# Performance work log

Measured on AMD Instinct MI355X. Metric: run time of the kernel, lower is better.

The kernel has to match this reference:

```python
import jax, jax.numpy as jnp
import numpy as np

DIM = 640
HEADS = 8
HEAD_DIM = 80
CROSS = 768
FF_INNER = 4 * DIM  # 2560
EPS = 1e-5
SCALE = HEAD_DIM ** -0.5


def _ln(x, w, b):
    m = jnp.mean(x, axis=-1, keepdims=True)
    v = jnp.var(x, axis=-1, keepdims=True)
    return (x - m) * jax.lax.rsqrt(v + EPS) * w + b


def _split_heads(x):  # [B,S,D] -> [B,H,S,dh]
    B, S, D = x.shape
    return x.reshape(B, S, HEADS, D // HEADS).transpose(0, 2, 1, 3)


def _merge_heads(x):  # [B,H,S,dh] -> [B,S,D]
    B, H, S, dh = x.shape
    return x.transpose(0, 2, 1, 3).reshape(B, S, H * dh)


def _mha(q, k, v):
    # q:[B,S,D] k,v:[B,Skv,D]
    qh, kh, vh = _split_heads(q), _split_heads(k), _split_heads(v)
    scores = jnp.einsum('bhqd,bhkd->bhqk', qh, kh) * SCALE
    probs = jax.nn.softmax(scores, axis=-1)
    out = jnp.einsum('bhqk,bhkd->bhqd', probs, vh)
    return _merge_heads(out)


def _forward(hidden_states, encoder_hidden_states, video_length, p):
    BF, S, D = hidden_states.shape
    f = video_length
    b = BF // f

    # ---- attn1: sparse causal self-attention ----
    x = _ln(hidden_states, p['ln1_w'], p['ln1_b'])
    q = x @ p['q1']
    k = x @ p['k1']
    v = x @ p['v1']
    former = jnp.concatenate([jnp.zeros((1,), jnp.int32), jnp.arange(f - 1, dtype=jnp.int32)])
    def gather_kv(t):  # [BF,S,D] -> [BF,2S,D]
        t = t.reshape(b, f, S, D)
        first = jnp.broadcast_to(t[:, 0:1], (b, f, S, D))
        prev = t[:, former]
        return jnp.concatenate([first, prev], axis=2).reshape(BF, 2 * S, D)
    k = gather_kv(k)
    v = gather_kv(v)
    attn1 = _mha(q, k, v) @ p['o1_w'] + p['o1_b']
    hidden_states = attn1 + hidden_states

    # ---- attn2: cross attention to text ----
    x = _ln(hidden_states, p['ln2_w'], p['ln2_b'])
    q = x @ p['q2']
    k = encoder_hidden_states @ p['k2']
    v = encoder_hidden_states @ p['v2']
    attn2 = _mha(q, k, v) @ p['o2_w'] + p['o2_b']
    hidden_states = attn2 + hidden_states

    # ---- feed-forward (geglu) ----
    x = _ln(hidden_states, p['ln3_w'], p['ln3_b'])
    proj = x @ p['ff_w1'] + p['ff_b1']
    h, gate = jnp.split(proj, 2, axis=-1)
    ff = (h * jax.nn.gelu(gate)) @ p['ff_w2'] + p['ff_b2']
    return ff + hidden_states


def setup_inputs() -> dict:
    key = jax.random.key(0)
    ks = jax.random.split(key, 20)
    s = lambda i, shape, scale=0.02: jax.random.normal(ks[i], shape, jnp.float32) * scale
    inp = {
        'hidden_states': jax.random.normal(ks[0], (8, 1024, DIM), jnp.float32),
        'encoder_hidden_states': jax.random.normal(ks[1], (8, 77, CROSS), jnp.float32),
        'video_length': 8,
        'ln1_w': jnp.ones((DIM,)), 'ln1_b': jnp.zeros((DIM,)),
        'q1': s(2, (DIM, DIM)), 'k1': s(3, (DIM, DIM)), 'v1': s(4, (DIM, DIM)),
        'o1_w': s(5, (DIM, DIM)), 'o1_b': jnp.zeros((DIM,)),
        'ln2_w': jnp.ones((DIM,)), 'ln2_b': jnp.zeros((DIM,)),
        'q2': s(6, (DIM, DIM)), 'k2': s(7, (CROSS, DIM)), 'v2': s(8, (CROSS, DIM)),
        'o2_w': s(9, (DIM, DIM)), 'o2_b': jnp.zeros((DIM,)),
        'ln3_w': jnp.ones((DIM,)), 'ln3_b': jnp.zeros((DIM,)),
        'ff_w1': s(10, (DIM, 2 * FF_INNER)), 'ff_b1': jnp.zeros((2 * FF_INNER,)),
        'ff_w2': s(11, (FF_INNER, DIM)), 'ff_b2': jnp.zeros((DIM,)),
    }
    return inp


def reference(hidden_states, encoder_hidden_states, video_length,
              ln1_w, ln1_b, q1, k1, v1, o1_w, o1_b,
              ln2_w, ln2_b, q2, k2, v2, o2_w, o2_b,
              ln3_w, ln3_b, ff_w1, ff_b1, ff_w2, ff_b2):
    p = dict(ln1_w=ln1_w, ln1_b=ln1_b, q1=q1, k1=k1, v1=v1, o1_w=o1_w, o1_b=o1_b,
             ln2_w=ln2_w, ln2_b=ln2_b, q2=q2, k2=k2, v2=v2, o2_w=o2_w, o2_b=o2_b,
             ln3_w=ln3_w, ln3_b=ln3_b, ff_w1=ff_w1, ff_b1=ff_b1, ff_w2=ff_w2, ff_b2=ff_b2)
    return _forward(hidden_states, encoder_hidden_states, video_length, p)
```

## Files before the change

kernel.cpp:

```cpp
#include <hip/hip_runtime.h>
#include <stdint.h>

#define TOK   8192
#define DIM   640
#define HEADS 8
#define HD    80
#define SEQ   1024
#define CROSS 768
#define ETOK  616
#define FFI   2560
#define SCALE 0.11180339887498949f

typedef unsigned short u16;
typedef unsigned int   u32;

using bf8   = __attribute__((ext_vector_type(8))) short;
using f32x4 = __attribute__((ext_vector_type(4))) float;

struct __align__(16) U4 { u32 x, y, z, w; };
struct __align__(8)  U2 { u32 x, y; };

__device__ __forceinline__ float bf2f(u16 u){
  union { u32 i; float f; } v; v.i = ((u32)u) << 16; return v.f;
}
__device__ __forceinline__ u16 f2bf(float f){
  union { float f; u32 i; } v; v.f = f;
  u32 r = v.i + 0x7fffu + ((v.i >> 16) & 1u);
  return (u16)(r >> 16);
}
__device__ __forceinline__ u32 cvtpk_bf16(float lo, float hi){
  u32 r; asm("v_cvt_pk_bf16_f32 %0, %1, %2" : "=v"(r) : "v"(lo), "v"(hi)); return r;
}
__device__ __forceinline__ float gelu_t(float x){
  float y = 0.7978845608028654f * (x + 0.044715f * x * x * x);
  float e = __expf(2.f * y);
  return 0.5f * x * (2.f - 2.f / (e + 1.f));
}

__device__ __forceinline__ void gl2lds16(const u16* g, u16* l){
  __builtin_amdgcn_global_load_lds(
      (const __attribute__((address_space(1))) void*)g,
      (__attribute__((address_space(3))) void*)l, 16, 0, 0);
}

__global__ void zero_k(u16* p){ p[threadIdx.x] = 0; }

struct CvtJob  { const float* s; u16* d; int n; };
struct CvtJobs { CvtJob j[11]; };
__global__ __launch_bounds__(256) void cvt_all(CvtJobs jobs)
{
  const CvtJob jb = jobs.j[blockIdx.y];
  for (long i = (long)blockIdx.x*256 + threadIdx.x; i < jb.n; i += (long)gridDim.x*256)
    jb.d[i] = f2bf(jb.s[i]);
}

struct TJob  { const float* s; u16* d; int R, C, srcLd, dstLd; };
struct TJobs { TJob j[10]; };
__global__ __launch_bounds__(256) void transpose_tiled(TJobs jobs)
{
  const TJob jb = jobs.j[blockIdx.y];
  const int tilesC = jb.C >> 6;
  const int nt = (jb.R >> 6) * tilesC;
  if ((int)blockIdx.x >= nt) return;
  const int tr = (blockIdx.x / tilesC) << 6, tc = (blockIdx.x % tilesC) << 6;
  __shared__ u16 t[64][65];
  const int tid = threadIdx.x;
  const int rr = tid >> 3, c8 = (tid & 7) * 8;
  #pragma unroll
  for (int p = 0; p < 2; ++p){
    const int r = rr + p*32;
    const float* s = &jb.s[(long)(tr + r)*jb.srcLd + tc + c8];
    #pragma unroll
    for (int j = 0; j < 8; ++j) t[r][c8 + j] = f2bf(s[j]);
  }
  __syncthreads();
  #pragma unroll
  for (int p = 0; p < 2; ++p){
    const int c = rr + p*32;
    u16 tmp[8];
    #pragma unroll
    for (int j = 0; j < 8; ++j) tmp[j] = t[c8 + j][c];
    *(U4*)&jb.d[(long)(tc + c)*jb.dstLd + tr + c8] = *(U4*)tmp;
  }
}

__global__ __launch_bounds__(256) void transpose_tile(
    const u16* __restrict__ src, u16* __restrict__ dst,
    int srcLd, int dstLd)
{
  __shared__ u16 t[64][65];
  const int tr = blockIdx.y << 6, tc = blockIdx.x << 6;
  const int tid = threadIdx.x;
  const int rr = tid >> 3, c8 = (tid & 7) * 8;
  #pragma unroll
  for (int p = 0; p < 2; ++p){
    const int r = rr + p*32;
    U4 v = *(const U4*)&src[(long)(tr + r)*srcLd + tc + c8];
    const u16* pv = (const u16*)&v;
    #pragma unroll
    for (int j = 0; j < 8; ++j) t[r][c8 + j] = pv[j];
  }
  __syncthreads();
  #pragma unroll
  for (int p = 0; p < 2; ++p){
    const int c = rr + p*32;
    u16 tmp[8];
    #pragma unroll
    for (int j = 0; j < 8; ++j) tmp[j] = t[c8 + j][c];
    *(U4*)&dst[(long)(tc + c)*dstLd + tr + c8] = *(U4*)tmp;
  }
}

__global__ __launch_bounds__(256) void transpose_v2(
    const u16* __restrict__ src, u16* __restrict__ dst)
{
  int idx = blockIdx.x*256 + threadIdx.x;
  if (idx >= DIM*640) return;
  int d = idx / 640, c = idx - d*640;
  int g = c / 80, j = c - g*80;
  u16 v = 0;
  if (j < 77) v = src[(long)(g*77 + j)*(2*DIM) + DIM + d];
  dst[(long)d*640 + c] = v;
}

__global__ __launch_bounds__(256) void ln_k(
    const void* __restrict__ src, const u16* __restrict__ w,
    const u16* __restrict__ b, u16* __restrict__ dst, int srcf32)
{
  const int wave = threadIdx.x >> 6, lane = threadIdx.x & 63;
  const long row = (long)blockIdx.x*4 + wave;
  float x[10];
  if (srcf32){
    const float* s = (const float*)src + row*DIM;
    #pragma unroll
    for (int j = 0; j < 5; ++j){
      float2 v = *(const float2*)&s[lane*2 + j*128];
      x[j*2] = v.x; x[j*2+1] = v.y;
    }
  } else {
    const u16* s = (const u16*)src + row*DIM;
    #pragma unroll
    for (int j = 0; j < 5; ++j){
      u32 v = *(const u32*)&s[lane*2 + j*128];
      x[j*2]   = bf2f((u16)(v & 0xffffu));
      x[j*2+1] = bf2f((u16)(v >> 16));
    }
  }
  float sum = 0.f;
  #pragma unroll
  for (int i = 0; i < 10; ++i) sum += x[i];
  #pragma unroll
  for (int d = 1; d < 64; d <<= 1) sum += __shfl_xor(sum, d, 64);
  const float mean = sum * (1.f/DIM);
  float vq = 0.f;
  #pragma unroll
  for (int i = 0; i < 10; ++i){ float dd = x[i] - mean; vq += dd*dd; }
  #pragma unroll
  for (int d = 1; d < 64; d <<= 1) vq += __shfl_xor(vq, d, 64);
  const float rs = rsqrtf(vq * (1.f/DIM) + 1e-5f);
  u16* q = dst + row*DIM;
  #pragma unroll
  for (int j = 0; j < 5; ++j){
    const int off = lane*2 + j*128;
    u32 wv = *(const u32*)&w[off];
    u32 bv = *(const u32*)&b[off];
    float o0 = (x[j*2]   - mean)*rs*bf2f((u16)(wv & 0xffffu)) + bf2f((u16)(bv & 0xffffu));
    float o1 = (x[j*2+1] - mean)*rs*bf2f((u16)(wv >> 16))     + bf2f((u16)(bv >> 16));
    *(u32*)&q[off] = (u32)f2bf(o0) | ((u32)f2bf(o1) << 16);
  }
}

template<int BN>
__global__ __launch_bounds__(256) void gemm_bt(
    const u16* __restrict__ A, const u16* __restrict__ BT, void* __restrict__ C,
    int M, int N, int K, int lda, int ldb, int ldc,
    const u16* __restrict__ bias, const void* __restrict__ res, int ldr,
    int resf32, int outf32)
{
  constexpr int NT  = BN/32;
  constexpr int BCH = BN/16;
  constexpr int BPW = BCH/4;
  __shared__ __align__(16) u16 sA[2][8*512];
  __shared__ __align__(16) u16 sB[2][BCH*512];
  const int tid  = threadIdx.x;
  const int wave = tid >> 6, lane = tid & 63;
  const int quad = lane >> 4, l16 = lane & 15;
  const int m0 = blockIdx.y * 128, n0 = blockIdx.x * BN;
  const int wm = (wave >> 1) * 64, wn = (wave & 1) * (BN/2);
  const int srow = lane & 15;
  const int scol = (lane >> 4) * 8;

  long aoff[2];
  #pragma unroll
  for (int i = 0; i < 2; ++i){
    int r = m0 + (wave*2 + i)*16 + srow;
    r = r < M ? r : M - 1;
    aoff[i] = (long)r*lda + scol;
  }
  long boff[BPW];
  #pragma unroll
  for (int i = 0; i < BPW; ++i){
    int r = n0 + (wave*BPW + i)*16 + srow;
    boff[i] = (long)r*ldb + scol;
  }

  f32x4 acc[4][NT] = {};
  #pragma unroll
  for (int i = 0; i < 2; ++i)   gl2lds16(&A[aoff[i]],  &sA[0][(wave*2 + i)*512]);
  #pragma unroll
  for (int i = 0; i < BPW; ++i) gl2lds16(&BT[boff[i]], &sB[0][(wave*BPW + i)*512]);
  __syncthreads();

  int cur = 0;
  for (int k0 = 0; ; ){
    const int kn = k0 + 32;
    if (kn < K){
      #pragma unroll
      for (int i = 0; i < 2; ++i)   gl2lds16(&A[aoff[i] + kn],  &sA[cur^1][(wave*2 + i)*512]);
      #pragma unroll
      for (int i = 0; i < BPW; ++i) gl2lds16(&BT[boff[i] + kn], &sB[cur^1][(wave*BPW + i)*512]);
    }
    bf8 a[4], b[NT];
    #pragma unroll
    for (int mt = 0; mt < 4; ++mt)  a[mt] = *(const bf8*)&sA[cur][((wm>>4) + mt)*512 + lane*8];
    #pragma unroll
    for (int nt = 0; nt < NT; ++nt) b[nt] = *(const bf8*)&sB[cur][((wn>>4) + nt)*512 + lane*8];
    #pragma unroll
    for (int mt = 0; mt < 4; ++mt)
      #pragma unroll
      for (int nt = 0; nt < NT; ++nt)
        acc[mt][nt] = __builtin_amdgcn_mfma_f32_16x16x32_bf16(a[mt], b[nt], acc[mt][nt], 0, 0, 0);
    k0 = kn;
    if (k0 >= K) break;
    __syncthreads();
    cur ^= 1;
  }
  #pragma unroll
  for (int mt = 0; mt < 4; ++mt){
    const int rl = wm + mt*16 + quad*4;
    #pragma unroll
    for (int nt = 0; nt < NT; ++nt){
      const int col = n0 + wn + nt*16 + l16;
      float bv = bias ? bf2f(bias[col]) : 0.f;
      #pragma unroll
      for (int r = 0; r < 4; ++r){
        int row = m0 + rl + r;
        if (row < M){
          float v = acc[mt][nt][r] + bv;
          if (res) v += resf32 ? ((const float*)res)[(long)row*ldr + col]
                               : bf2f(((const u16*)res)[(long)row*ldr + col]);
          if (outf32) ((float*)C)[(long)row*ldc + col] = v;
          else        ((u16*)C) [(long)row*ldc + col] = f2bf(v);
        }
      }
    }
  }
}

__global__ __launch_bounds__(256) void gemm_geglu(
    const u16* __restrict__ A, const u16* __restrict__ W, u16* __restrict__ C,
    const u16* __restrict__ bias)
{
  __shared__ __align__(16) u16 sA[2][8*512];
  __shared__ __align__(16) u16 sH[2][4*512];
  __shared__ __align__(16) u16 sG[2][4*512];
  const int tid  = threadIdx.x;
  const int wave = tid >> 6, lane = tid & 63;
  const int quad = lane >> 4, l16 = lane & 15;
  const int m0 = blockIdx.y * 128, n0 = blockIdx.x * 64;
  const int wm = (wave >> 1) * 64, wn = (wave & 1) * 32;
  const int srow = lane & 15;
  const int scol = (lane >> 4) * 8;

  long aoff[2];
  #pragma unroll
  for (int i = 0; i < 2; ++i)
    aoff[i] = (long)(m0 + (wave*2 + i)*16 + srow)*DIM + scol;
  const long hoff = (long)(n0 + wave*16 + srow)*DIM + scol;
  const long goff = (long)(FFI + n0 + wave*16 + srow)*DIM + scol;

  f32x4 ah[4][2] = {}, ag[4][2] = {};
  #pragma unroll
  for (int i = 0; i < 2; ++i) gl2lds16(&A[aoff[i]], &sA[0][(wave*2 + i)*512]);
  gl2lds16(&W[hoff], &sH[0][wave*512]);
  gl2lds16(&W[goff], &sG[0][wave*512]);
  __syncthreads();

  int cur = 0;
  for (int k0 = 0; ; ){
    const int kn = k0 + 32;
    if (kn < DIM){
      #pragma unroll
      for (int i = 0; i < 2; ++i) gl2lds16(&A[aoff[i] + kn], &sA[cur^1][(wave*2 + i)*512]);
      gl2lds16(&W[hoff + kn], &sH[cur^1][wave*512]);
      gl2lds16(&W[goff + kn], &sG[cur^1][wave*512]);
    }
    bf8 a[4];
    #pragma unroll
    for (int mt = 0; mt < 4; ++mt) a[mt] = *(const bf8*)&sA[cur][((wm>>4) + mt)*512 + lane*8];
    #pragma unroll
    for (int nt = 0; nt < 2; ++nt){
      bf8 bh = *(const bf8*)&sH[cur][((wn>>4) + nt)*512 + lane*8];
      bf8 bg = *(const bf8*)&sG[cur][((wn>>4) + nt)*512 + lane*8];
      #pragma unroll
      for (int mt = 0; mt < 4; ++mt){
        ah[mt][nt] = __builtin_amdgcn_mfma_f32_16x16x32_bf16(a[mt], bh, ah[mt][nt], 0, 0, 0);
        ag[mt][nt] = __builtin_amdgcn_mfma_f32_16x16x32_bf16(a[mt], bg, ag[mt][nt], 0, 0, 0);
      }
    }
    k0 = kn;
    if (k0 >= DIM) break;
    __syncthreads();
    cur ^= 1;
  }
  #pragma unroll
  for (int mt = 0; mt < 4; ++mt){
    const int rl = wm + mt*16 + quad*4;
    #pragma unroll
    for (int nt = 0; nt < 2; ++nt){
      const int col = n0 + wn + nt*16 + l16;
      const float bh = bf2f(bias[col]);
      const float bg = bf2f(bias[FFI + col]);
      #pragma unroll
      for (int r = 0; r < 4; ++r){
        int row = m0 + rl + r;
        float h = ah[mt][nt][r] + bh;
        float g = ag[mt][nt][r] + bg;
        C[(long)row*FFI + col] = f2bf(h * gelu_t(g));
      }
    }
  }
}

template<int MODE>
__global__ __launch_bounds__(256) void attn_k(
    const u16* __restrict__ qbuf, const u16* __restrict__ kbuf,
    const u16* __restrict__ vT, u16* __restrict__ out,
    const u16* __restrict__ zblk)
{
  constexpr int QLD  = MODE ? DIM      : 3*DIM;
  constexpr int KLD  = MODE ? 2*DIM    : 3*DIM;
  constexpr int KCOL = MODE ? 0        : DIM;
  constexpr int VLD  = MODE ? DIM      : TOK;
  constexpr int NK   = MODE ? 77       : 2*SEQ;
  constexpr int NCH  = MODE ? 3        : 64;
  constexpr float C1   = SCALE * 1.4426950408889634f;
  constexpr float THRR = 8.0f / C1;

  const int qt = blockIdx.x, h = blockIdx.y, g = blockIdx.z;
  const int tid = threadIdx.x, wave = tid >> 6, lane = tid & 63;
  const int quad = lane >> 4, l16 = lane & 15;

  __shared__ __align__(16) u16 Kb[2][6*512];
  __shared__ __align__(16) u16 Vb[2][5*512];
  __shared__ __align__(16) u16 Ps[4][16*40];

  const int qrow0 = g*SEQ + qt*64;
  bf8 qf[3];
  {
    const long qbase = (long)(qrow0 + wave*16 + l16)*QLD + h*HD;
    #pragma unroll
    for (int ks = 0; ks < 3; ++ks){
      const int d = ks*32 + quad*8;
      const u16* src = (d < HD) ? &qbuf[qbase + d] : zblk;
      qf[ks] = *(const bf8*)src;
    }
  }

  const int former = (g == 0) ? 0 : (g - 1);

  const bool kc1v = (wave < 2);
  const int  vc0  = (wave + 2) & 3;
  const bool vc1v = (wave == 2);

  long ko[2] = {0,0}, koB[2] = {0,0}, vo[2] = {0,0}, voB[2] = {0,0};
  bool koob[2];
  #pragma unroll
  for (int j = 0; j < 2; ++j){
    const int ci = wave + 4*j;
    const int ck = ci/3, ks = ci - ck*3;
    const int d = ks*32 + quad*8;
    koob[j] = (d >= HD);
    if (MODE == 0){
      const int dcl = koob[j] ? 0 : d;
      const int row = ck*16 + l16;
      ko[j]  = (long)row*KLD + KCOL + h*HD + dcl;
      koB[j] = ko[j] + (long)former*SEQ*KLD;
    }
  }
  if (MODE == 0){
    vo[0]  = (long)(h*HD + vc0*16 + l16)*VLD + quad*8;
    vo[1]  = (long)(h*HD + 64    + l16)*VLD + quad*8;
    voB[0] = vo[0] + (long)former*SEQ;
    voB[1] = vo[1] + (long)former*SEQ;
  }

  auto stageM0 = [&](int buf){
    gl2lds16(koob[0] ? zblk : &kbuf[ko[0]], &Kb[buf][(wave)*512]);
    if (kc1v) gl2lds16(koob[1] ? zblk : &kbuf[ko[1]], &Kb[buf][(wave+4)*512]);
    gl2lds16(&vT[vo[0]], &Vb[buf][vc0*512]);
    if (vc1v) gl2lds16(&vT[vo[1]], &Vb[buf][4*512]);
    ko[0] += 32L*KLD; ko[1] += 32L*KLD;
    vo[0] += 32; vo[1] += 32;
  };
  auto stageM1 = [&](int c, int buf){
    #pragma unroll
    for (int ci = 0; ci < 6; ++ci){
      if ((ci & 3) == wave){
        const int ck = ci / 3, ks = ci % 3;
        const int d  = ks*32 + quad*8;
        const int rl = ck*16 + l16;
        int j = c*32 + rl; j = j < NK ? j : NK-1;
        const u16* src = (d < HD) ? &kbuf[((long)g*77 + j)*KLD + KCOL + h*HD + d] : zblk;
        gl2lds16(src, &Kb[buf][ci*512]);
      }
    }
    #pragma unroll
    for (int vi = 0; vi < 5; ++vi){
      if (((vi + 2) & 3) == wave){
        const int dd = vi*16 + l16;
        int key = c*32 + quad*8;
        const u16* src = (key < 80) ? &vT[(long)(h*HD + dd)*VLD + g*80 + key] : zblk;
        gl2lds16(src, &Vb[buf][vi*512]);
      }
    }
  };

  f32x4 o[5] = {};
  float mrun = -1e30f, lrun = 0.f, nmc = 0.f;

  if (MODE == 0) stageM0(0); else stageM1(0, 0);
  __syncthreads();
  int cur = 0;

  for (int c = 0; c < NCH; ++c){
    if (c + 1 < NCH){
      if (MODE == 0){
        if (c + 1 == 32){
          ko[0] = koB[0]; ko[1] = koB[1];
          vo[0] = voB[0]; vo[1] = voB[1];
        }
        stageM0(cur ^ 1);
      } else {
        stageM1(c + 1, cur ^ 1);
      }
    }

    f32x4 s0 = {}, s1 = {};
    #pragma unroll
    for (int ks = 0; ks < 3; ++ks){
      bf8 kf0 = *(const bf8*)&Kb[cur][ks*512     + lane*8];
      bf8 kf1 = *(const bf8*)&Kb[cur][(3+ks)*512 + lane*8];
      s0 = __builtin_amdgcn_mfma_f32_16x16x32_bf16(kf0, qf[ks], s0, 0, 0, 0);
      s1 = __builtin_amdgcn_mfma_f32_16x16x32_bf16(kf1, qf[ks], s1, 0, 0, 0);
    }

    if (MODE == 1){
      const int kg = c*32 + quad*4;
      #pragma unroll
      for (int r = 0; r < 4; ++r){
        if (kg + r >= NK)      s0[r] = -1e30f;
        if (kg + 16 + r >= NK) s1[r] = -1e30f;
      }
    }
    float mxs = fmaxf(fmaxf(fmaxf(s0[0],s0[1]), fmaxf(s0[2],s0[3])),
                      fmaxf(fmaxf(s1[0],s1[1]), fmaxf(s1[2],s1[3])));
    if (!__all(mxs - mrun <= THRR)){
      float mx = fmaxf(mxs, __shfl_xor(mxs, 16, 64));
      mx = fmaxf(mx, __shfl_xor(mx, 32, 64));
      float mn = fmaxf(mrun, mx);
      float al = exp2f((mrun - mn)*C1);
      mrun = mn; nmc = -mrun*C1;
      lrun *= al;
      float a0 = __shfl(al, quad*4 + 0, 16);
      float a1 = __shfl(al, quad*4 + 1, 16);
      float a2 = __shfl(al, quad*4 + 2, 16);
      float a3 = __shfl(al, quad*4 + 3, 16);
      #pragma unroll
      for (int dt = 0; dt < 5; ++dt){
        o[dt][0] *= a0; o[dt][1] *= a1; o[dt][2] *= a2; o[dt][3] *= a3;
      }
    }
    #pragma unroll
    for (int r = 0; r < 4; ++r){
      s0[r] = exp2f(__builtin_fmaf(s0[r], C1, nmc));
      s1[r] = exp2f(__builtin_fmaf(s1[r], C1, nmc));
    }
    lrun += ((s0[0]+s0[1])+(s0[2]+s0[3])) + ((s1[0]+s1[1])+(s1[2]+s1[3]));

    U2 w01, w23;
    w01.x = cvtpk_bf16(s0[0], s0[1]);  w01.y = cvtpk_bf16(s0[2], s0[3]);
    w23.x = cvtpk_bf16(s1[0], s1[1]);  w23.y = cvtpk_bf16(s1[2], s1[3]);
    U2* pr = (U2*)&Ps[wave][l16*40];
    pr[quad]     = w01;
    pr[4 + quad] = w23;
    asm volatile("s_waitcnt lgkmcnt(0)" ::: "memory");
    __builtin_amdgcn_sched_barrier(0);
    bf8 pf = *(const bf8*)&Ps[wave][l16*40 + quad*8];
    #pragma unroll
    for (int dt = 0; dt < 5; ++dt){
      bf8 vf = *(const bf8*)&Vb[cur][dt*512 + lane*8];
      o[dt] = __builtin_amdgcn_mfma_f32_16x16x32_bf16(pf, vf, o[dt], 0, 0, 0);
    }
    __syncthreads();
    cur ^= 1;
  }

  lrun += __shfl_xor(lrun, 16, 64);
  lrun += __shfl_xor(lrun, 32, 64);

  float linv[4];
  #pragma unroll
  for (int r = 0; r < 4; ++r)
    linv[r] = __builtin_amdgcn_rcpf(__shfl(lrun, quad*4 + r, 16));
  const int orow0 = qrow0 + wave*16 + quad*4;
  #pragma unroll
  for (int dt = 0; dt < 5; ++dt){
    const int col = h*HD + dt*16 + l16;
    #pragma unroll
    for (int r = 0; r < 4; ++r)
      out[(long)(orow0 + r)*DIM + col] = f2bf(o[dt][r] * linv[r]);
  }
}

extern "C" void kernel_launch(void* const* d_in, const int* in_sizes, int n_in,
                              void* d_out, int out_size, void* d_ws, size_t ws_size,
                              hipStream_t stream)
{
  const float* hidden = (const float*)d_in[0];
  const float* enc    = (const float*)d_in[1];
  const float* ln1w = (const float*)d_in[3],  *ln1b = (const float*)d_in[4];
  const float* q1   = (const float*)d_in[5],  *k1   = (const float*)d_in[6];
  const float* v1   = (const float*)d_in[7],  *o1w  = (const float*)d_in[8];
  const float* o1b  = (const float*)d_in[9];
  const float* ln2w = (const float*)d_in[10], *ln2b = (const float*)d_in[11];
  const float* q2   = (const float*)d_in[12], *k2   = (const float*)d_in[13];
  const float* v2   = (const float*)d_in[14], *o2w  = (const float*)d_in[15];
  const float* o2b  = (const float*)d_in[16];
  const float* ln3w = (const float*)d_in[17], *ln3b = (const float*)d_in[18];
  const float* fw1  = (const float*)d_in[19], *fb1  = (const float*)d_in[20];
  const float* fw2  = (const float*)d_in[21], *fb2  = (const float*)d_in[22];

  u16* ws = (u16*)d_ws;
  u16* Wqkv1T = ws;
  u16* o1T    = Wqkv1T + 1920*640;
  u16* q2T    = o1T    + 640*640;
  u16* Wkv2T  = q2T    + 640*640;
  u16* o2T    = Wkv2T  + 1280*768;
  u16* W1T    = o2T    + 640*640;
  u16* W2T    = W1T    + 5120*640;
  u16* xbuf   = W2T    + 640*2560;
  u16* qkv1   = xbuf   + (size_t)TOK*DIM;
  u16* v1T    = qkv1   + (size_t)TOK*3*DIM;
  u16* ffin   = qkv1;
  u16* attnb  = v1T    + (size_t)DIM*TOK;
  u16* hid2   = attnb  + (size_t)TOK*DIM;
  u16* hid3   = hid2   + (size_t)TOK*DIM;
  u16* q2buf  = hid3   + (size_t)TOK*DIM;
  u16* kv2    = q2buf  + (size_t)TOK*DIM;
  u16* v2T    = kv2    + (size_t)ETOK*2*DIM;
  u16* encm   = v2T    + 640*640 + 64;
  u16* bln1w  = encm   + (size_t)ETOK*CROSS;
  u16* bln1b  = bln1w + DIM;
  u16* bo1b   = bln1b + DIM;
  u16* bln2w  = bo1b  + DIM;
  u16* bln2b  = bln2w + DIM;
  u16* bo2b   = bln2b + DIM;
  u16* bln3w  = bo2b  + DIM;
  u16* bln3b  = bln3w + DIM;
  u16* bfb2   = bln3b + DIM;
  u16* bfb1   = bfb2  + DIM;
  u16* zblk   = bfb1  + 2*FFI;
  u16* wsend  = zblk  + 64;
  const size_t needed = ((size_t)(wsend - ws) + 64) * 2;
  if (ws_size < needed) return;

  dim3 blk(256);
  zero_k<<<1, 64, 0, stream>>>(zblk);

  CvtJobs jobs;
  jobs.j[0]  = { enc,  encm,  ETOK*CROSS };
  jobs.j[1]  = { ln1w, bln1w, DIM };
  jobs.j[2]  = { ln1b, bln1b, DIM };
  jobs.j[3]  = { o1b,  bo1b,  DIM };
  jobs.j[4]  = { ln2w, bln2w, DIM };
  jobs.j[5]  = { ln2b, bln2b, DIM };
  jobs.j[6]  = { o2b,  bo2b,  DIM };
  jobs.j[7]  = { ln3w, bln3w, DIM };
  jobs.j[8]  = { ln3b, bln3b, DIM };
  jobs.j[9]  = { fb2,  bfb2,  DIM };
  jobs.j[10] = { fb1,  bfb1,  2*FFI };
  cvt_all<<<dim3(64,11), blk, 0, stream>>>(jobs);

  TJobs tj;
  tj.j[0] = { q1,  Wqkv1T,            640, 640,  640,  640 };
  tj.j[1] = { k1,  Wqkv1T + 640*640,  640, 640,  640,  640 };
  tj.j[2] = { v1,  Wqkv1T + 1280*640, 640, 640,  640,  640 };
  tj.j[3] = { o1w, o1T,               640, 640,  640,  640 };
  tj.j[4] = { q2,  q2T,               640, 640,  640,  640 };
  tj.j[5] = { k2,  Wkv2T,             768, 640,  640,  768 };
  tj.j[6] = { v2,  Wkv2T + 640*768,   768, 640,  640,  768 };
  tj.j[7] = { o2w, o2T,               640, 640,  640,  640 };
  tj.j[8] = { fw1, W1T,               640, 5120, 5120, 640 };
  tj.j[9] = { fw2, W2T,               2560,640,  640,  2560 };
  transpose_tiled<<<dim3(800,10), blk, 0, stream>>>(tj);

  ln_k<<<TOK/4, blk, 0, stream>>>(hidden, bln1w, bln1b, xbuf, 1);
  gemm_bt<128><<<dim3(15,64), blk, 0, stream>>>(xbuf, Wqkv1T, qkv1,
      TOK, 3*DIM, DIM, DIM, DIM, 3*DIM, nullptr, nullptr, 0, 0, 0);
  transpose_tile<<<dim3(10,128), blk, 0, stream>>>(qkv1 + 2*DIM, v1T, 3*DIM, TOK);
  attn_k<0><<<dim3(16,8,8), blk, 0, stream>>>(qkv1, qkv1, v1T, attnb, zblk);
  gemm_bt<64><<<dim3(10,64), blk, 0, stream>>>(attnb, o1T, hid2,
      TOK, DIM, DIM, DIM, DIM, DIM, bo1b, hidden, DIM, 1, 0);

  ln_k<<<TOK/4, blk, 0, stream>>>(hid2, bln2w, bln2b, xbuf, 0);
  gemm_bt<64><<<dim3(10,64), blk, 0, stream>>>(xbuf, q2T, q2buf,
      TOK, DIM, DIM, DIM, DIM, DIM, nullptr, nullptr, 0, 0, 0);
  gemm_bt<64><<<dim3(20,5), blk, 0, stream>>>(encm, Wkv2T, kv2,
      ETOK, 2*DIM, CROSS, CROSS, CROSS, 2*DIM, nullptr, nullptr, 0, 0, 0);
  transpose_v2<<<dim3((DIM*640 + 255)/256), blk, 0, stream>>>(kv2, v2T);
  attn_k<1><<<dim3(16,8,8), blk, 0, stream>>>(q2buf, kv2, v2T, attnb, zblk);
  gemm_bt<64><<<dim3(10,64), blk, 0, stream>>>(attnb, o2T, hid3,
      TOK, DIM, DIM, DIM, DIM, DIM, bo2b, hid2, DIM, 0, 0);

  ln_k<<<TOK/4, blk, 0, stream>>>(hid3, bln3w, bln3b, xbuf, 0);
  gemm_geglu<<<dim3(40,64), blk, 0, stream>>>(xbuf, W1T, ffin, bfb1);
  gemm_bt<64><<<dim3(10,64), blk, 0, stream>>>(ffin, W2T, d_out,
      TOK, DIM, FFI, FFI, FFI, DIM, bfb2, hid3, DIM, 0, 1);
}
```

Baseline: 669.9 us.

## Triple-buffer GEMM LDS staging with explicit vmcnt waits and single barrier

After: 664.9 us. No clear change (-0.7%).

```diff
diff --git a/kernel.cpp b/kernel.cpp
--- a/kernel.cpp
+++ b/kernel.cpp
@@ -180,8 +180,9 @@
   constexpr int NT  = BN/32;
   constexpr int BCH = BN/16;
   constexpr int BPW = BCH/4;
-  __shared__ __align__(16) u16 sA[2][8*512];
-  __shared__ __align__(16) u16 sB[2][BCH*512];
+  constexpr int LPW = 2 + BPW;
+  __shared__ __align__(16) u16 sA[3][8*512];
+  __shared__ __align__(16) u16 sB[3][BCH*512];
   const int tid  = threadIdx.x;
   const int wave = tid >> 6, lane = tid & 63;
   const int quad = lane >> 4, l16 = lane & 15;
@@ -204,21 +205,29 @@
     boff[i] = (long)r*ldb + scol;
   }
 
+  auto stage = [&](int ks, int buf){
+    const int kk = ks*32;
+    #pragma unroll
+    for (int i = 0; i < 2; ++i)   gl2lds16(&A[aoff[i] + kk],  &sA[buf][(wave*2 + i)*512]);
+    #pragma unroll
+    for (int i = 0; i < BPW; ++i) gl2lds16(&BT[boff[i] + kk], &sB[buf][(wave*BPW + i)*512]);
+  };
+
+  const int NS = K >> 5;
   f32x4 acc[4][NT] = {};
-  #pragma unroll
-  for (int i = 0; i < 2; ++i)   gl2lds16(&A[aoff[i]],  &sA[0][(wave*2 + i)*512]);
-  #pragma unroll
-  for (int i = 0; i < BPW; ++i) gl2lds16(&BT[boff[i]], &sB[0][(wave*BPW + i)*512]);
-  __syncthreads();
+  stage(0, 0);
+  if (NS > 1) stage(1, 1);
 
   int cur = 0;
-  for (int k0 = 0; ; ){
-    const int kn = k0 + 32;
-    if (kn < K){
-      #pragma unroll
-      for (int i = 0; i < 2; ++i)   gl2lds16(&A[aoff[i] + kn],  &sA[cur^1][(wave*2 + i)*512]);
-      #pragma unroll
-      for (int i = 0; i < BPW; ++i) gl2lds16(&BT[boff[i] + kn], &sB[cur^1][(wave*BPW + i)*512]);
+  for (int ks = 0; ks < NS; ++ks){
+    if (ks < NS - 1) asm volatile("s_waitcnt vmcnt(%0)" :: "n"(LPW) : "memory");
+    else             asm volatile("s_waitcnt vmcnt(0)" ::: "memory");
+    __builtin_amdgcn_sched_barrier(0);
+    __builtin_amdgcn_s_barrier();
+    __builtin_amdgcn_sched_barrier(0);
+    if (ks + 2 < NS){
+      int nbuf = cur + 2; if (nbuf >= 3) nbuf -= 3;
+      stage(ks + 2, nbuf);
     }
     bf8 a[4], b[NT];
     #pragma unroll
@@ -230,10 +239,7 @@
       #pragma unroll
       for (int nt = 0; nt < NT; ++nt)
         acc[mt][nt] = __builtin_amdgcn_mfma_f32_16x16x32_bf16(a[mt], b[nt], acc[mt][nt], 0, 0, 0);
-    k0 = kn;
-    if (k0 >= K) break;
-    __syncthreads();
-    cur ^= 1;
+    cur = (cur == 2) ? 0 : cur + 1;
   }
   #pragma unroll
   for (int mt = 0; mt < 4; ++mt){
@@ -261,9 +267,10 @@
     const u16* __restrict__ A, const u16* __restrict__ W, u16* __restrict__ C,
     const u16* __restrict__ bias)
 {
-  __shared__ __align__(16) u16 sA[2][8*512];
-  __shared__ __align__(16) u16 sH[2][4*512];
-  __shared__ __align__(16) u16 sG[2][4*512];
+  constexpr int LPW = 4;
+  __shared__ __align__(16) u16 sA[3][8*512];
+  __shared__ __align__(16) u16 sH[3][4*512];
+  __shared__ __align__(16) u16 sG[3][4*512];
   const int tid  = threadIdx.x;
   const int wave = tid >> 6, lane = tid & 63;
   const int quad = lane >> 4, l16 = lane & 15;
@@ -279,21 +286,29 @@
   const long hoff = (long)(n0 + wave*16 + srow)*DIM + scol;
   const long goff = (long)(FFI + n0 + wave*16 + srow)*DIM + scol;
 
+  auto stage = [&](int ks, int buf){
+    const int kk = ks*32;
+    #pragma unroll
+    for (int i = 0; i < 2; ++i) gl2lds16(&A[aoff[i] + kk], &sA[buf][(wave*2 + i)*512]);
+    gl2lds16(&W[hoff + kk], &sH[buf][wave*512]);
+    gl2lds16(&W[goff + kk], &sG[buf][wave*512]);
+  };
+
+  constexpr int NS = DIM/32;
   f32x4 ah[4][2] = {}, ag[4][2] = {};
-  #pragma unroll
-  for (int i = 0; i < 2; ++i) gl2lds16(&A[aoff[i]], &sA[0][(wave*2 + i)*512]);
-  gl2lds16(&W[hoff], &sH[0][wave*512]);
-  gl2lds16(&W[goff], &sG[0][wave*512]);
-  __syncthreads();
+  stage(0, 0);
+  stage(1, 1);
 
   int cur = 0;
-  for (int k0 = 0; ; ){
-    const int kn = k0 + 32;
-    if (kn < DIM){
-      #pragma unroll
-      for (int i = 0; i < 2; ++i) gl2lds16(&A[aoff[i] + kn], &sA[cur^1][(wave*2 + i)*512]);
-      gl2lds16(&W[hoff + kn], &sH[cur^1][wave*512]);
-      gl2lds16(&W[goff + kn], &sG[cur^1][wave*512]);
+  for (int ks = 0; ks < NS; ++ks){
+    if (ks < NS - 1) asm volatile("s_waitcnt vmcnt(%0)" :: "n"(LPW) : "memory");
+    else             asm volatile("s_waitcnt vmcnt(0)" ::: "memory");
+    __builtin_amdgcn_sched_barrier(0);
+    __builtin_amdgcn_s_barrier();
+    __builtin_amdgcn_sched_barrier(0);
+    if (ks + 2 < NS){
+      int nbuf = cur + 2; if (nbuf >= 3) nbuf -= 3;
+      stage(ks + 2, nbuf);
     }
     bf8 a[4];
     #pragma unroll
@@ -308,10 +323,7 @@
         ag[mt][nt] = __builtin_amdgcn_mfma_f32_16x16x32_bf16(a[mt], bg, ag[mt][nt], 0, 0, 0);
       }
     }
-    k0 = kn;
-    if (k0 >= DIM) break;
-    __syncthreads();
-    cur ^= 1;
+    cur = (cur == 2) ? 0 : cur + 1;
   }
   #pragma unroll
   for (int mt = 0; mt < 4; ++mt){
```
